# Optimization experiments

Measured on AMD Instinct MI355X. Metric: run time of the kernel, lower is better.

The kernel has to match this reference:

```python
import jax, jax.numpy as jnp
import numpy as np

B, N, F = 8, 8192, 64
NPOINT, NSAMPLE = 2048, 32
RADIUS = 0.2
MLP = [64, 64, 128]
EPS = 1e-5
SLOPE = 0.2


def fps(pts_t, npoint):
    """Furthest point sampling. pts_t: (B,N,3) -> (B,npoint) int32 indices."""
    b, n, _ = pts_t.shape
    def body(carry, _):
        dist, far = carry
        centroid = jnp.take_along_axis(pts_t, far[:, None, None], axis=1)  # (B,1,3)
        d = jnp.sum((pts_t - centroid) ** 2, axis=-1)                      # (B,N)
        dist = jnp.minimum(dist, d)
        return (dist, jnp.argmax(dist, axis=-1).astype(jnp.int32)), far
    init = (jnp.full((b, n), 1e10, pts_t.dtype), jnp.zeros((b,), jnp.int32))
    _, idxs = jax.lax.scan(body, init, None, length=npoint)
    return jnp.transpose(idxs)  # (B,npoint)


def ball_query(pts_t, q_t, radius, k):
    """pts_t: (B,N,3), q_t: (B,S,3) -> (B,S,k) int32; first in-ball index fills empty slots."""
    n = pts_t.shape[1]
    d = (jnp.sum(q_t ** 2, -1, keepdims=True) + jnp.sum(pts_t ** 2, -1)[:, None, :]
         - 2.0 * jnp.einsum('bsc,bnc->bsn', q_t, pts_t))
    idx = jnp.where(d < radius * radius, jnp.arange(n, dtype=jnp.int32)[None, None, :], n)
    idx = -jax.lax.top_k(-idx, k)[0]  # k smallest indices, ascending order
    first = idx[:, :, :1]
    return jnp.where(idx == n, first, idx)


def _layer(x, w, b, g, bb, m, v):
    # 1x1 conv + BatchNorm(eval) + LeakyReLU(0.2); x: (B,S,K,Cin) -> (B,S,K,Cout)
    y = jnp.einsum('bskc,oc->bsko', x, w) + b
    y = (y - m) * (g * jax.lax.rsqrt(v + EPS)) + bb
    return jnp.where(y > 0, y, SLOPE * y)


def _forward(features, points, params):
    pts_t = jnp.transpose(points, (0, 2, 1))  # (B,N,3)
    fidx = fps(jax.lax.stop_gradient(pts_t), NPOINT)                    # (B,S)
    new_xyz_t = jnp.take_along_axis(pts_t, fidx[:, :, None], axis=1)    # (B,S,3)
    idx = ball_query(jax.lax.stop_gradient(pts_t), jax.lax.stop_gradient(new_xyz_t), RADIUS, NSAMPLE)
    gather = jax.vmap(lambda p, i: p[i])
    grouped_xyz = gather(pts_t, idx) - new_xyz_t[:, :, None, :]         # (B,S,K,3)
    grouped_feat = gather(jnp.transpose(features, (0, 2, 1)), idx)      # (B,S,K,F)
    x = jnp.concatenate([grouped_xyz, grouped_feat], axis=-1)           # (B,S,K,3+F)
    for (w, b, g, bb, m, v) in params:
        x = _layer(x, w, b, g, bb, m, v)
    new_features = jnp.transpose(jnp.max(x, axis=2), (0, 2, 1))         # (B,mlp[-1],S)
    new_xyz = jnp.transpose(new_xyz_t, (0, 2, 1))                       # (B,3,S)
    return new_features, new_xyz


def setup_inputs() -> dict:
    key = jax.random.key(0)
    ks = jax.random.split(key, 32)
    inp = {
        'features': jax.random.normal(ks[0], (B, F, N), jnp.float32),
        'points': jax.random.uniform(ks[1], (B, 3, N), jnp.float32),
    }
    chans = [F + 3] + MLP
    j = 2
    for i in range(len(MLP)):
        cin, cout = chans[i], chans[i + 1]
        inp[f'w{i+1}'] = jax.random.normal(ks[j], (cout, cin), jnp.float32) / np.sqrt(cin).astype(np.float32); j += 1
        inp[f'b{i+1}'] = jax.random.normal(ks[j], (cout,), jnp.float32) * 0.1; j += 1
        inp[f'g{i+1}'] = jax.random.uniform(ks[j], (cout,), jnp.float32, 0.5, 1.5); j += 1
        inp[f'bb{i+1}'] = jax.random.normal(ks[j], (cout,), jnp.float32) * 0.1; j += 1
        inp[f'm{i+1}'] = jax.random.normal(ks[j], (cout,), jnp.float32) * 0.1; j += 1
        inp[f'v{i+1}'] = jax.random.uniform(ks[j], (cout,), jnp.float32, 0.5, 1.5); j += 1
    return inp


def reference(features, points, w1, b1, g1, bb1, m1, v1, w2, b2, g2, bb2, m2, v2, w3, b3, g3, bb3, m3, v3):
    params = [(w1, b1, g1, bb1, m1, v1), (w2, b2, g2, bb2, m2, v2), (w3, b3, g3, bb3, m3, v3)]
    return _forward(features, points, params)
```

## Files before the change

### kernel.cpp

```cpp
#include <hip/hip_runtime.h>
#include <cstdint>
#include <cstddef>

#define NBATCH  8
#define NPTS    8192
#define NFEAT   64
#define NPOINT  2048
#define NSAMPLE 32

__global__ void prep_kernel(const float* __restrict__ w1, const float* __restrict__ b1,
                            const float* __restrict__ g1, const float* __restrict__ bb1,
                            const float* __restrict__ m1, const float* __restrict__ v1,
                            const float* __restrict__ w2, const float* __restrict__ b2,
                            const float* __restrict__ g2, const float* __restrict__ bb2,
                            const float* __restrict__ m2, const float* __restrict__ v2,
                            const float* __restrict__ w3, const float* __restrict__ b3,
                            const float* __restrict__ g3, const float* __restrict__ bb3,
                            const float* __restrict__ m3, const float* __restrict__ v3,
                            float* __restrict__ wbuf) {
    int i = blockIdx.x * 256 + threadIdx.x;
    if (i < 4288) {
        int o = i & 63, c = i >> 6;
        float s = g1[o] / sqrtf(v1[o] + 1e-5f);
        wbuf[i] = w1[o * 67 + c] * s;
    } else if (i < 4352) {
        int o = i - 4288;
        float s = g1[o] / sqrtf(v1[o] + 1e-5f);
        wbuf[i] = (b1[o] - m1[o]) * s + bb1[o];
    } else if (i < 8448) {
        int j = i - 4352; int o = j & 63, c = j >> 6;
        float s = g2[o] / sqrtf(v2[o] + 1e-5f);
        wbuf[i] = w2[o * 64 + c] * s;
    } else if (i < 8512) {
        int o = i - 8448;
        float s = g2[o] / sqrtf(v2[o] + 1e-5f);
        wbuf[i] = (b2[o] - m2[o]) * s + bb2[o];
    } else if (i < 16704) {
        int j = i - 8512; int o = j & 127, c = j >> 7;
        float s = g3[o] / sqrtf(v3[o] + 1e-5f);
        wbuf[i] = w3[o * 64 + c] * s;
    } else if (i < 16832) {
        int o = i - 16704;
        float s = g3[o] / sqrtf(v3[o] + 1e-5f);
        wbuf[i] = (b3[o] - m3[o]) * s + bb3[o];
    }
}

__global__ __launch_bounds__(512) void fps_kernel(const float* __restrict__ points,
                                                  int* __restrict__ fidx) {
    const int b = blockIdx.x;
    const int tid = threadIdx.x;
    const int lane = tid & 63;
    const float* __restrict__ pxg = points + (size_t)b * 3 * NPTS;
    const float* __restrict__ pyg = pxg + NPTS;
    const float* __restrict__ pzg = pyg + NPTS;

    float px[16], py[16], pz[16], dd[16];
#pragma unroll
    for (int j = 0; j < 16; ++j) {
        int n = tid + 512 * j;
        px[j] = pxg[n]; py[j] = pyg[n]; pz[j] = pzg[n];
        dd[j] = 1e10f;
    }
    __shared__ float pv[2][8];
    __shared__ int   pi[2][8];
    if (tid == 0) fidx[b * NPOINT + 0] = 0;
    int w = 0;
    for (int i = 1; i < NPOINT; ++i) {
        const float cx = pxg[w], cy = pyg[w], cz = pzg[w];
        float bestd = -1.0f; int besti = 0;
#pragma unroll
        for (int j = 0; j < 16; ++j) {
            float dx = __fsub_rn(px[j], cx);
            float dy = __fsub_rn(py[j], cy);
            float dz = __fsub_rn(pz[j], cz);
            float d  = __fadd_rn(__fadd_rn(__fmul_rn(dx, dx), __fmul_rn(dy, dy)),
                                 __fmul_rn(dz, dz));
            float nd = fminf(dd[j], d);
            dd[j] = nd;
            bool better = (nd > bestd);
            bestd = better ? nd : bestd;
            besti = better ? (tid + 512 * j) : besti;
        }
#pragma unroll
        for (int off = 32; off >= 1; off >>= 1) {
            float od = __shfl_down(bestd, off);
            int   oi = __shfl_down(besti, off);
            bool take = (od > bestd) || (od == bestd && oi < besti);
            bestd = take ? od : bestd;
            besti = take ? oi : besti;
        }
        const int par = i & 1;
        if (lane == 0) { pv[par][tid >> 6] = bestd; pi[par][tid >> 6] = besti; }
        __syncthreads();
        float fd = (lane < 8) ? pv[par][lane] : -1.0f;
        int   fi = (lane < 8) ? pi[par][lane] : 0x7fffffff;
#pragma unroll
        for (int off = 4; off >= 1; off >>= 1) {
            float od = __shfl_down(fd, off);
            int   oi = __shfl_down(fi, off);
            bool take = (od > fd) || (od == fd && oi < fi);
            fd = take ? od : fd;
            fi = take ? oi : fi;
        }
        w = __shfl(fi, 0);
        if (tid == 0) fidx[b * NPOINT + i] = w;
    }
}

__global__ __launch_bounds__(256) void bq_kernel(const float* __restrict__ points,
                                                 const int* __restrict__ fidx,
                                                 int* __restrict__ ballidx,
                                                 float* __restrict__ out_xyz) {
    const int lane = threadIdx.x & 63;
    const int gw = (blockIdx.x << 2) + (threadIdx.x >> 6);
    const int b = gw >> 11;
    const int q = gw & 2047;
    const float* __restrict__ pxg = points + (size_t)b * 3 * NPTS;
    const float* __restrict__ pyg = pxg + NPTS;
    const float* __restrict__ pzg = pyg + NPTS;
    const int qi = fidx[b * NPOINT + q];
    const float qx = pxg[qi], qy = pyg[qi], qz = pzg[qi];
    const float qq = __fadd_rn(__fadd_rn(__fmul_rn(qx, qx), __fmul_rn(qy, qy)),
                               __fmul_rn(qz, qz));
    int* __restrict__ out = ballidx + ((size_t)(b * NPOINT + q)) * NSAMPLE;
    int have = 0;
    int first = -1;
    for (int base = 0; base < NPTS && have < NSAMPLE; base += 64) {
        const int n = base + lane;
        float x = pxg[n], y = pyg[n], z = pzg[n];
        float pp = __fadd_rn(__fadd_rn(__fmul_rn(x, x), __fmul_rn(y, y)), __fmul_rn(z, z));
        float qp = __builtin_fmaf(qz, z, __builtin_fmaf(qy, y, __fmul_rn(qx, x)));
        float d  = __fsub_rn(__fadd_rn(qq, pp), __fmul_rn(2.0f, qp));
        bool inb = d < 0.04f;
        unsigned long long mask = __ballot(inb);
        if (mask) {
            if (first < 0) first = base + __ffsll(mask) - 1;
            if (inb) {
                int slot = have + (int)__popcll(mask & ((1ull << lane) - 1ull));
                if (slot < NSAMPLE) out[slot] = n;
            }
            have += (int)__popcll(mask);
        }
    }
    for (int s = have + lane; s < NSAMPLE; s += 64) out[s] = first;
    if (lane == 0) {
        float* o0 = out_xyz + (size_t)b * 3 * NPOINT + q;
        o0[0] = qx; o0[NPOINT] = qy; o0[2 * NPOINT] = qz;
    }
}

#define XS 36
__global__ __launch_bounds__(256) void mlp_kernel(const float* __restrict__ feats,
                                                  const float* __restrict__ points,
                                                  const int* __restrict__ fidx,
                                                  const int* __restrict__ ballidx,
                                                  const float* __restrict__ wbuf,
                                                  float* __restrict__ out) {
    __shared__ float xT[67 * XS];
    __shared__ float yA[64 * XS];
    __shared__ float wl[8192];
    __shared__ float bl[128];
    __shared__ int   il[32];
    __shared__ float qv[3];
    const int tid = threadIdx.x;
    const int bq = blockIdx.x;
    const int b = bq >> 11, q = bq & 2047;
    const float* __restrict__ pb = points + (size_t)b * 3 * NPTS;

    if (tid < 32) il[tid] = ballidx[((size_t)(b * NPOINT + q)) * NSAMPLE + tid];
    if (tid < 3)  qv[tid] = pb[(size_t)tid * NPTS + fidx[b * NPOINT + q]];
    for (int i = tid; i < 4288; i += 256) wl[i] = wbuf[i];
    if (tid < 64) bl[tid] = wbuf[4288 + tid];
    __syncthreads();

    if (tid < 32) {
        int n = il[tid];
        xT[0 * XS + tid] = pb[n] - qv[0];
        xT[1 * XS + tid] = pb[NPTS + n] - qv[1];
        xT[2 * XS + tid] = pb[2 * NPTS + n] - qv[2];
    }
    {
        int k = tid & 31, fg = tid >> 5;
        int n = il[k];
        const float* fb = feats + ((size_t)b * NFEAT + fg * 8) * NPTS + n;
#pragma unroll
        for (int u = 0; u < 8; ++u) xT[(3 + fg * 8 + u) * XS + k] = fb[(size_t)u * NPTS];
    }
    __syncthreads();

    const int o = tid & 63, kb = tid >> 6;
    float acc[8];
#pragma unroll
    for (int j = 0; j < 8; ++j) acc[j] = 0.f;
    for (int c = 0; c < 67; ++c) {
        float wv = wl[c * 64 + o];
        const float4* xp = (const float4*)&xT[c * XS + kb * 8];
        float4 a0 = xp[0], a1 = xp[1];
        acc[0] = fmaf(wv, a0.x, acc[0]); acc[1] = fmaf(wv, a0.y, acc[1]);
        acc[2] = fmaf(wv, a0.z, acc[2]); acc[3] = fmaf(wv, a0.w, acc[3]);
        acc[4] = fmaf(wv, a1.x, acc[4]); acc[5] = fmaf(wv, a1.y, acc[5]);
        acc[6] = fmaf(wv, a1.z, acc[6]); acc[7] = fmaf(wv, a1.w, acc[7]);
    }
    {
        float t = bl[o];
#pragma unroll
        for (int j = 0; j < 8; ++j) {
            float y = acc[j] + t;
            y = y > 0.f ? y : 0.2f * y;
            yA[o * XS + kb * 8 + j] = y;
        }
    }
    __syncthreads();
    for (int i = tid; i < 4096; i += 256) wl[i] = wbuf[4352 + i];
    if (tid < 64) bl[tid] = wbuf[8448 + tid];
    __syncthreads();

#pragma unroll
    for (int j = 0; j < 8; ++j) acc[j] = 0.f;
    for (int c = 0; c < 64; ++c) {
        float wv = wl[c * 64 + o];
        const float4* xp = (const float4*)&yA[c * XS + kb * 8];
        float4 a0 = xp[0], a1 = xp[1];
        acc[0] = fmaf(wv, a0.x, acc[0]); acc[1] = fmaf(wv, a0.y, acc[1]);
        acc[2] = fmaf(wv, a0.z, acc[2]); acc[3] = fmaf(wv, a0.w, acc[3]);
        acc[4] = fmaf(wv, a1.x, acc[4]); acc[5] = fmaf(wv, a1.y, acc[5]);
        acc[6] = fmaf(wv, a1.z, acc[6]); acc[7] = fmaf(wv, a1.w, acc[7]);
    }
    {
        float t = bl[o];
#pragma unroll
        for (int j = 0; j < 8; ++j) {
            float y = acc[j] + t;
            y = y > 0.f ? y : 0.2f * y;
            xT[o * XS + kb * 8 + j] = y;
        }
    }
    __syncthreads();
    for (int i = tid; i < 8192; i += 256) wl[i] = wbuf[8512 + i];
    if (tid < 128) bl[tid] = wbuf[16704 + tid];
    __syncthreads();

    const int o3 = tid & 127, kb3 = tid >> 7;
    float a3[16];
#pragma unroll
    for (int j = 0; j < 16; ++j) a3[j] = 0.f;
    for (int c = 0; c < 64; ++c) {
        float wv = wl[c * 128 + o3];
        const float4* xp = (const float4*)&xT[c * XS + kb3 * 16];
        float4 x0 = xp[0], x1 = xp[1], x2 = xp[2], x3 = xp[3];
        a3[0]  = fmaf(wv, x0.x, a3[0]);  a3[1]  = fmaf(wv, x0.y, a3[1]);
        a3[2]  = fmaf(wv, x0.z, a3[2]);  a3[3]  = fmaf(wv, x0.w, a3[3]);
        a3[4]  = fmaf(wv, x1.x, a3[4]);  a3[5]  = fmaf(wv, x1.y, a3[5]);
        a3[6]  = fmaf(wv, x1.z, a3[6]);  a3[7]  = fmaf(wv, x1.w, a3[7]);
        a3[8]  = fmaf(wv, x2.x, a3[8]);  a3[9]  = fmaf(wv, x2.y, a3[9]);
        a3[10] = fmaf(wv, x2.z, a3[10]); a3[11] = fmaf(wv, x2.w, a3[11]);
        a3[12] = fmaf(wv, x3.x, a3[12]); a3[13] = fmaf(wv, x3.y, a3[13]);
        a3[14] = fmaf(wv, x3.z, a3[14]); a3[15] = fmaf(wv, x3.w, a3[15]);
    }
    {
        float t = bl[o3];
        float m = -3.4e38f;
#pragma unroll
        for (int j = 0; j < 16; ++j) {
            float y = a3[j] + t;
            y = y > 0.f ? y : 0.2f * y;
            m = fmaxf(m, y);
        }
        yA[o3 * 2 + kb3] = m;
    }
    __syncthreads();
    if (tid < 128) {
        float r = fmaxf(yA[tid * 2], yA[tid * 2 + 1]);
        out[((size_t)b * 128 + tid) * NPOINT + q] = r;
    }
}

extern "C" void kernel_launch(void* const* d_in, const int* in_sizes, int n_in,
                              void* d_out, int out_size, void* d_ws, size_t ws_size,
                              hipStream_t stream) {
    (void)in_sizes; (void)n_in; (void)out_size; (void)ws_size;
    const float* feats  = (const float*)d_in[0];
    const float* points = (const float*)d_in[1];
    const float* w1  = (const float*)d_in[2];
    const float* b1  = (const float*)d_in[3];
    const float* g1  = (const float*)d_in[4];
    const float* bb1 = (const float*)d_in[5];
    const float* m1  = (const float*)d_in[6];
    const float* v1  = (const float*)d_in[7];
    const float* w2  = (const float*)d_in[8];
    const float* b2  = (const float*)d_in[9];
    const float* g2  = (const float*)d_in[10];
    const float* bb2 = (const float*)d_in[11];
    const float* m2  = (const float*)d_in[12];
    const float* v2  = (const float*)d_in[13];
    const float* w3  = (const float*)d_in[14];
    const float* b3  = (const float*)d_in[15];
    const float* g3  = (const float*)d_in[16];
    const float* bb3 = (const float*)d_in[17];
    const float* m3  = (const float*)d_in[18];
    const float* v3  = (const float*)d_in[19];

    float* out = (float*)d_out;
    char*  ws  = (char*)d_ws;
    int*   fidx    = (int*)ws;
    int*   ballidx = (int*)(ws + 65536);
    float* wbuf    = (float*)(ws + 65536 + 2097152);
    float* out_xyz = out + (size_t)NBATCH * 128 * NPOINT;

    hipLaunchKernelGGL(prep_kernel, dim3(66), dim3(256), 0, stream,
                       w1, b1, g1, bb1, m1, v1, w2, b2, g2, bb2, m2, v2,
                       w3, b3, g3, bb3, m3, v3, wbuf);
    hipLaunchKernelGGL(fps_kernel, dim3(NBATCH), dim3(512), 0, stream, points, fidx);
    hipLaunchKernelGGL(bq_kernel, dim3(16384 / 4), dim3(256), 0, stream,
                       points, fidx, ballidx, out_xyz);
    hipLaunchKernelGGL(mlp_kernel, dim3(NBATCH * NPOINT), dim3(256), 0, stream,
                       feats, points, fidx, ballidx, wbuf, out);
}
```

Measured before the change: 3.449 ms.

## Bin FPS points into a spatial grid in LDS and prune cells with bounding spheres

Result: slower. 9.987 ms (+189.6%).

```diff
diff --git a/kernel.cpp b/kernel.cpp
--- a/kernel.cpp
+++ b/kernel.cpp
@@ -46,65 +46,144 @@
     }
 }
 
-__global__ __launch_bounds__(512) void fps_kernel(const float* __restrict__ points,
-                                                  int* __restrict__ fidx) {
+__global__ __launch_bounds__(512, 2) void fps_kernel(const float* __restrict__ points,
+                                                     int* __restrict__ fidx) {
     const int b = blockIdx.x;
     const int tid = threadIdx.x;
     const int lane = tid & 63;
+    const int wv = tid >> 6;
     const float* __restrict__ pxg = points + (size_t)b * 3 * NPTS;
     const float* __restrict__ pyg = pxg + NPTS;
     const float* __restrict__ pzg = pyg + NPTS;
 
-    float px[16], py[16], pz[16], dd[16];
+    __shared__ float sx[NPTS], sy[NPTS], sz[NPTS];
+    __shared__ float sdd[NPTS];
+    __shared__ unsigned short sorig[NPTS];
+    __shared__ int cnt[512];
+    __shared__ int cellstart[513];
+    __shared__ float wbv[8];
+    __shared__ int   wbo[8];
+    __shared__ float cs[3];
+
+    float px[16], py[16], pz[16];
+    cnt[tid] = 0;
 #pragma unroll
     for (int j = 0; j < 16; ++j) {
         int n = tid + 512 * j;
         px[j] = pxg[n]; py[j] = pyg[n]; pz[j] = pzg[n];
-        dd[j] = 1e10f;
-    }
-    __shared__ float pv[2][8];
-    __shared__ int   pi[2][8];
-    if (tid == 0) fidx[b * NPOINT + 0] = 0;
-    int w = 0;
+    }
+    __syncthreads();
+#pragma unroll
+    for (int j = 0; j < 16; ++j) {
+        int cxi = min((int)(px[j] * 8.0f), 7);
+        int cyi = min((int)(py[j] * 8.0f), 7);
+        int czi = min((int)(pz[j] * 8.0f), 7);
+        atomicAdd(&cnt[(cxi << 6) | (cyi << 3) | czi], 1);
+    }
+    __syncthreads();
+    if (tid < 64) {
+        int base = tid * 8;
+        int loc[8]; int s = 0;
+#pragma unroll
+        for (int k = 0; k < 8; ++k) { loc[k] = cnt[base + k]; s += loc[k]; }
+        int inc = s;
+#pragma unroll
+        for (int off = 1; off < 64; off <<= 1) {
+            int t = __shfl_up(inc, off);
+            if (lane >= off) inc += t;
+        }
+        int run = inc - s;
+#pragma unroll
+        for (int k = 0; k < 8; ++k) { cellstart[base + k] = run; run += loc[k]; }
+        if (tid == 63) cellstart[512] = run;
+    }
+    __syncthreads();
+    cnt[tid] = cellstart[tid];
+    __syncthreads();
+#pragma unroll
+    for (int j = 0; j < 16; ++j) {
+        int n = tid + 512 * j;
+        int cxi = min((int)(px[j] * 8.0f), 7);
+        int cyi = min((int)(py[j] * 8.0f), 7);
+        int czi = min((int)(pz[j] * 8.0f), 7);
+        int pos = atomicAdd(&cnt[(cxi << 6) | (cyi << 3) | czi], 1);
+        sx[pos] = px[j]; sy[pos] = py[j]; sz[pos] = pz[j];
+        sorig[pos] = (unsigned short)n;
+        sdd[pos] = 1e10f;
+    }
+    __syncthreads();
+    const int p0 = cellstart[tid], p1 = cellstart[tid + 1];
+    float ccx = 0.f, ccy = 0.f, ccz = 0.f, rr = 0.f;
+    float bestv = -1.0f; int besto = 0x7fffffff; int bestp = p0;
+    if (p1 > p0) {
+        float mnx = 1e30f, mny = 1e30f, mnz = 1e30f;
+        float mxx = -1e30f, mxy = -1e30f, mxz = -1e30f;
+        for (int p = p0; p < p1; ++p) {
+            float x = sx[p], y = sy[p], z = sz[p];
+            mnx = fminf(mnx, x); mxx = fmaxf(mxx, x);
+            mny = fminf(mny, y); mxy = fmaxf(mxy, y);
+            mnz = fminf(mnz, z); mxz = fmaxf(mxz, z);
+            int o = (int)sorig[p];
+            if (o < besto) { besto = o; bestp = p; }
+        }
+        ccx = (mnx + mxx) * 0.5f; ccy = (mny + mxy) * 0.5f; ccz = (mnz + mxz) * 0.5f;
+        float hx = (mxx - mnx) * 0.5f, hy = (mxy - mny) * 0.5f, hz = (mxz - mnz) * 0.5f;
+        rr = sqrtf(hx * hx + hy * hy + hz * hz) * 1.0001f + 1e-7f;
+        bestv = 1e10f;
+    }
+    float cx = pxg[0], cy = pyg[0], cz = pzg[0];
+    if (tid == 0) fidx[b * NPOINT] = 0;
+
     for (int i = 1; i < NPOINT; ++i) {
-        const float cx = pxg[w], cy = pyg[w], cz = pzg[w];
-        float bestd = -1.0f; int besti = 0;
-#pragma unroll
-        for (int j = 0; j < 16; ++j) {
-            float dx = __fsub_rn(px[j], cx);
-            float dy = __fsub_rn(py[j], cy);
-            float dz = __fsub_rn(pz[j], cz);
-            float d  = __fadd_rn(__fadd_rn(__fmul_rn(dx, dx), __fmul_rn(dy, dy)),
-                                 __fmul_rn(dz, dz));
-            float nd = fminf(dd[j], d);
-            dd[j] = nd;
-            bool better = (nd > bestd);
-            bestd = better ? nd : bestd;
-            besti = better ? (tid + 512 * j) : besti;
-        }
-#pragma unroll
-        for (int off = 32; off >= 1; off >>= 1) {
-            float od = __shfl_down(bestd, off);
-            int   oi = __shfl_down(besti, off);
-            bool take = (od > bestd) || (od == bestd && oi < besti);
-            bestd = take ? od : bestd;
-            besti = take ? oi : besti;
-        }
-        const int par = i & 1;
-        if (lane == 0) { pv[par][tid >> 6] = bestd; pi[par][tid >> 6] = besti; }
+        bool active = false;
+        if (p1 > p0) {
+            float ddx = cx - ccx, ddy = cy - ccy, ddz = cz - ccz;
+            float D = ddx * ddx + ddy * ddy + ddz * ddz;
+            float lb = sqrtf(D) - rr;
+            active = !(lb > 1e-3f && lb * lb * 0.999f > bestv);
+        }
+        if (active) {
+            float bv = -1.0f; int bo = 0x7fffffff; int bp = p0;
+            for (int p = p0; p < p1; ++p) {
+                float dx = __fsub_rn(sx[p], cx);
+                float dy = __fsub_rn(sy[p], cy);
+                float dz = __fsub_rn(sz[p], cz);
+                float d  = __fadd_rn(__fadd_rn(__fmul_rn(dx, dx), __fmul_rn(dy, dy)),
+                                     __fmul_rn(dz, dz));
+                float nd = fminf(sdd[p], d);
+                sdd[p] = nd;
+                int o = (int)sorig[p];
+                bool take = (nd > bv) || (nd == bv && o < bo);
+                bv = take ? nd : bv; bo = take ? o : bo; bp = take ? p : bp;
+            }
+            bestv = bv; besto = bo; bestp = bp;
+        }
+        unsigned long long act = __ballot(active);
+        if (act) {
+            float v = bestv; int o = besto;
+#pragma unroll
+            for (int off = 32; off >= 1; off >>= 1) {
+                float ov = __shfl_down(v, off);
+                int   oo = __shfl_down(o, off);
+                bool take = (ov > v) || (ov == v && oo < o);
+                v = take ? ov : v; o = take ? oo : o;
+            }
+            if (lane == 0) { wbv[wv] = v; wbo[wv] = o; }
+        }
         __syncthreads();
-        float fd = (lane < 8) ? pv[par][lane] : -1.0f;
-        int   fi = (lane < 8) ? pi[par][lane] : 0x7fffffff;
-#pragma unroll
-        for (int off = 4; off >= 1; off >>= 1) {
-            float od = __shfl_down(fd, off);
-            int   oi = __shfl_down(fi, off);
-            bool take = (od > fd) || (od == fd && oi < fi);
-            fd = take ? od : fd;
-            fi = take ? oi : fi;
-        }
-        w = __shfl(fi, 0);
-        if (tid == 0) fidx[b * NPOINT + i] = w;
+        float M = wbv[0]; int I = wbo[0];
+#pragma unroll
+        for (int k = 1; k < 8; ++k) {
+            float v = wbv[k]; int o = wbo[k];
+            bool take = (v > M) || (v == M && o < I);
+            M = take ? v : M; I = take ? o : I;
+        }
+        if (bestv == M && besto == I) {
+            cs[0] = sx[bestp]; cs[1] = sy[bestp]; cs[2] = sz[bestp];
+            fidx[b * NPOINT + i] = I;
+        }
+        __syncthreads();
+        cx = cs[0]; cy = cs[1]; cz = cs[2];
     }
 }
 
```

## Restructure FPS reduction with DPP argmax, carried coordinates, and 4-wave blocks

Applied to the files above, without the earlier changes.

After: 3.710 ms. +7.6%, slower.

```diff
diff --git a/kernel.cpp b/kernel.cpp
--- a/kernel.cpp
+++ b/kernel.cpp
@@ -46,65 +46,87 @@
     }
 }
 
-__global__ __launch_bounds__(512) void fps_kernel(const float* __restrict__ points,
-                                                  int* __restrict__ fidx) {
+template <int CTRL>
+__device__ __forceinline__ int dpp_mov(int x) {
+    return __builtin_amdgcn_update_dpp(x, x, CTRL, 0xF, 0xF, false);
+}
+
+#define DPP_ARGMAX_STEP(CTRL)                                               \
+    do {                                                                    \
+        float vv = __int_as_float(dpp_mov<CTRL>(__float_as_int(v)));        \
+        int   oo = dpp_mov<CTRL>(o);                                        \
+        float xx = __int_as_float(dpp_mov<CTRL>(__float_as_int(wx)));       \
+        float yy = __int_as_float(dpp_mov<CTRL>(__float_as_int(wy)));       \
+        float zz = __int_as_float(dpp_mov<CTRL>(__float_as_int(wz)));       \
+        bool tk = (vv > v) || (vv == v && oo < o);                          \
+        v = tk ? vv : v; o = tk ? oo : o;                                   \
+        wx = tk ? xx : wx; wy = tk ? yy : wy; wz = tk ? zz : wz;            \
+    } while (0)
+
+__global__ __launch_bounds__(256, 1) void fps_kernel(const float* __restrict__ points,
+                                                     int* __restrict__ fidx) {
     const int b = blockIdx.x;
     const int tid = threadIdx.x;
     const int lane = tid & 63;
+    const int wv = tid >> 6;
     const float* __restrict__ pxg = points + (size_t)b * 3 * NPTS;
     const float* __restrict__ pyg = pxg + NPTS;
     const float* __restrict__ pzg = pyg + NPTS;
 
-    float px[16], py[16], pz[16], dd[16];
-#pragma unroll
-    for (int j = 0; j < 16; ++j) {
-        int n = tid + 512 * j;
-        px[j] = pxg[n]; py[j] = pyg[n]; pz[j] = pzg[n];
-        dd[j] = 1e10f;
-    }
-    __shared__ float pv[2][8];
-    __shared__ int   pi[2][8];
-    if (tid == 0) fidx[b * NPOINT + 0] = 0;
-    int w = 0;
+    __shared__ float pvs[2][4], pxs[2][4], pys[2][4], pzs[2][4];
+    __shared__ int   pos[2][4];
+
+    float rx[32], ry[32], rz[32], rdd[32];
+#pragma unroll
+    for (int j = 0; j < 32; ++j) {
+        int n = tid + 256 * j;
+        rx[j] = pxg[n]; ry[j] = pyg[n]; rz[j] = pzg[n];
+        rdd[j] = 1e10f;
+    }
+    float cx = pxg[0], cy = pyg[0], cz = pzg[0];
+    if (tid == 0) fidx[b * NPOINT] = 0;
+
     for (int i = 1; i < NPOINT; ++i) {
-        const float cx = pxg[w], cy = pyg[w], cz = pzg[w];
-        float bestd = -1.0f; int besti = 0;
-#pragma unroll
-        for (int j = 0; j < 16; ++j) {
-            float dx = __fsub_rn(px[j], cx);
-            float dy = __fsub_rn(py[j], cy);
-            float dz = __fsub_rn(pz[j], cz);
+        float bv = -1.0f; int bj = 0;
+        float bx = 0.f, by = 0.f, bz = 0.f;
+#pragma unroll
+        for (int j = 0; j < 32; ++j) {
+            float dx = __fsub_rn(rx[j], cx);
+            float dy = __fsub_rn(ry[j], cy);
+            float dz = __fsub_rn(rz[j], cz);
             float d  = __fadd_rn(__fadd_rn(__fmul_rn(dx, dx), __fmul_rn(dy, dy)),
                                  __fmul_rn(dz, dz));
-            float nd = fminf(dd[j], d);
-            dd[j] = nd;
-            bool better = (nd > bestd);
-            bestd = better ? nd : bestd;
-            besti = better ? (tid + 512 * j) : besti;
-        }
-#pragma unroll
-        for (int off = 32; off >= 1; off >>= 1) {
-            float od = __shfl_down(bestd, off);
-            int   oi = __shfl_down(besti, off);
-            bool take = (od > bestd) || (od == bestd && oi < besti);
-            bestd = take ? od : bestd;
-            besti = take ? oi : besti;
-        }
+            float nd = fminf(rdd[j], d);
+            rdd[j] = nd;
+            bool take = (nd > bv);
+            bv = take ? nd : bv; bj = take ? j : bj;
+            bx = take ? rx[j] : bx; by = take ? ry[j] : by; bz = take ? rz[j] : bz;
+        }
+        float v = bv; int o = tid + (bj << 8);
+        float wx = bx, wy = by, wz = bz;
+        DPP_ARGMAX_STEP(0x111);
+        DPP_ARGMAX_STEP(0x112);
+        DPP_ARGMAX_STEP(0x114);
+        DPP_ARGMAX_STEP(0x118);
+        DPP_ARGMAX_STEP(0x142);
+        DPP_ARGMAX_STEP(0x143);
         const int par = i & 1;
-        if (lane == 0) { pv[par][tid >> 6] = bestd; pi[par][tid >> 6] = besti; }
+        if (lane == 63) {
+            pvs[par][wv] = v; pos[par][wv] = o;
+            pxs[par][wv] = wx; pys[par][wv] = wy; pzs[par][wv] = wz;
+        }
         __syncthreads();
-        float fd = (lane < 8) ? pv[par][lane] : -1.0f;
-        int   fi = (lane < 8) ? pi[par][lane] : 0x7fffffff;
-#pragma unroll
-        for (int off = 4; off >= 1; off >>= 1) {
-            float od = __shfl_down(fd, off);
-            int   oi = __shfl_down(fi, off);
-            bool take = (od > fd) || (od == fd && oi < fi);
-            fd = take ? od : fd;
-            fi = take ? oi : fi;
-        }
-        w = __shfl(fi, 0);
-        if (tid == 0) fidx[b * NPOINT + i] = w;
+        float M = pvs[par][0]; int I = pos[par][0];
+        float nx = pxs[par][0], ny = pys[par][0], nz = pzs[par][0];
+#pragma unroll
+        for (int k = 1; k < 4; ++k) {
+            float vk = pvs[par][k]; int ok = pos[par][k];
+            bool tk = (vk > M) || (vk == M && ok < I);
+            M = tk ? vk : M; I = tk ? ok : I;
+            nx = tk ? pxs[par][k] : nx; ny = tk ? pys[par][k] : ny; nz = tk ? pzs[par][k] : nz;
+        }
+        cx = nx; cy = ny; cz = nz;
+        if (tid == 0) fidx[b * NPOINT + i] = I;
     }
 }
 
@@ -311,7 +333,7 @@
     hipLaunchKernelGGL(prep_kernel, dim3(66), dim3(256), 0, stream,
                        w1, b1, g1, bb1, m1, v1, w2, b2, g2, bb2, m2, v2,
                        w3, b3, g3, bb3, m3, v3, wbuf);
-    hipLaunchKernelGGL(fps_kernel, dim3(NBATCH), dim3(512), 0, stream, points, fidx);
+    hipLaunchKernelGGL(fps_kernel, dim3(NBATCH), dim3(256), 0, stream, points, fidx);
     hipLaunchKernelGGL(bq_kernel, dim3(16384 / 4), dim3(256), 0, stream,
                        points, fidx, ballidx, out_xyz);
     hipLaunchKernelGGL(mlp_kernel, dim3(NBATCH * NPOINT), dim3(256), 0, stream,
```
